# Kernel tuning notes

Hardware: AMD Instinct MI355X
Metric: run time of the kernel (lower is better)

## Reference

```python
import math
import jax, jax.numpy as jnp
import numpy as np

# ---- static configuration (mirrors init_kwargs / chosen shapes) ----
MUL = 16          # multiplicity in "16x0e+16x1e+16x2e"
B_CFG = 64        # number of configurations in batch
N_ATOM = 64       # atoms per configuration
N_NODES = B_CFG * N_ATOM
N_PAIRS = B_CFG * N_ATOM * N_ATOM

# ---- real Wigner 3j symbols (e3nn convention), computed once in numpy ----
def _su2_cg(j1, m1, j2, m2, j3, m3):
    if m3 != m1 + m2:
        return 0.0
    f = math.factorial
    vmin = max(-j1 + j2 + m3, -j1 + m1, 0)
    vmax = min(j2 + j3 + m1, j3 - j1 + j2, j3 + m3)
    C = math.sqrt((2 * j3 + 1) * f(j3 + j1 - j2) * f(j3 - j1 + j2) * f(j1 + j2 - j3)
                  * f(j3 + m3) * f(j3 - m3)
                  / (f(j1 + j2 + j3 + 1) * f(j1 - m1) * f(j1 + m1) * f(j2 - m2) * f(j2 + m2)))
    S = 0.0
    for v in range(vmin, vmax + 1):
        S += (-1) ** (v + j2 + m2) * f(j2 + j3 + m1 - v) * f(j1 - m1 + v) / (
            f(v) * f(j3 - j1 + j2 - v) * f(j3 + m3 - v) * f(v + j1 - j2 - m3))
    return C * S

def _q_real_to_complex(l):
    q = np.zeros((2 * l + 1, 2 * l + 1), dtype=np.complex128)
    for m in range(-l, 0):
        q[l + m, l + abs(m)] = 1 / 2 ** 0.5
        q[l + m, l - abs(m)] = -1j / 2 ** 0.5
    q[l, l] = 1.0
    for m in range(1, l + 1):
        q[l + m, l + abs(m)] = (-1) ** m / 2 ** 0.5
        q[l + m, l - abs(m)] = 1j * (-1) ** m / 2 ** 0.5
    return (-1j) ** l * q

def _wigner_3j(l1, l2, l3):
    C = np.zeros((2 * l1 + 1, 2 * l2 + 1, 2 * l3 + 1))
    for m1 in range(-l1, l1 + 1):
        for m2 in range(-l2, l2 + 1):
            m3 = m1 + m2
            if abs(m3) <= l3:
                C[l1 + m1, l2 + m2, l3 + m3] = _su2_cg(l1, m1, l2, m2, l3, m3)
    Q1, Q2, Q3 = _q_real_to_complex(l1), _q_real_to_complex(l2), _q_real_to_complex(l3)
    Cr = np.einsum('ij,kl,mn,ikm->jln', Q1, Q2, np.conj(Q3), C.astype(np.complex128))
    assert np.abs(Cr.imag).max() < 1e-6
    Cr = Cr.real
    return Cr / np.linalg.norm(Cr)

# all CG paths (l1, l2, l_out) of the fully connected TP (0e+1e+2e)^2 -> 0e+1e+2e
PATHS = [(0, 0, 0), (1, 1, 0), (2, 2, 0),
         (0, 1, 1), (1, 0, 1), (1, 1, 1), (1, 2, 1), (2, 1, 1), (2, 2, 1),
         (0, 2, 2), (2, 0, 2), (1, 1, 2), (1, 2, 2), (2, 1, 2), (2, 2, 2)]
W3J = {p: _wigner_3j(*p) for p in set(PATHS)}
FAN = {lo: sum(1 for p in PATHS if p[2] == lo) * MUL * MUL for lo in (0, 1, 2)}
ALPHA = {lo: math.sqrt(2 * lo + 1) / math.sqrt(FAN[lo]) for lo in (0, 1, 2)}
# CartesianTensor('ij=ij') change of basis: x_ij = sum_{l,m} QCART[lm,i,j] * irreps[lm]
QCART = np.concatenate([math.sqrt(2 * l + 1) * np.transpose(_wigner_3j(1, 1, l), (2, 0, 1))
                        for l in (0, 1, 2)], axis=0)  # (9, 3, 3), orthonormal rows


def setup_inputs() -> dict:
    key = jax.random.key(0)
    k1, k2 = jax.random.split(key)
    node_feats = jax.random.normal(k1, (N_NODES, MUL * 9), dtype=jnp.float32)
    # layout: for each config, all (i, j) atom pairs with global node indices
    ii, jj = jnp.meshgrid(jnp.arange(N_ATOM, dtype=jnp.int32),
                          jnp.arange(N_ATOM, dtype=jnp.int32), indexing='ij')
    base = (jnp.arange(B_CFG, dtype=jnp.int32) * N_ATOM)[:, None, None]
    rows = (base + ii[None]).reshape(-1)
    cols = (base + jj[None]).reshape(-1)
    layout = jnp.stack([rows, cols], axis=1)  # (N_PAIRS, 2) int32
    tp_weights = jax.random.normal(k2, (len(PATHS), MUL, MUL), dtype=jnp.float32)
    return {'node_feats': node_feats, 'layout': layout, 'tp_weights': tp_weights}


def _split(x):
    # (E, MUL*9) -> {l: (E, MUL, 2l+1)} in irreps order 16x0e | 16x1e | 16x2e
    E = x.shape[0]
    return {0: x[:, :MUL].reshape(E, MUL, 1),
            1: x[:, MUL:4 * MUL].reshape(E, MUL, 3),
            2: x[:, 4 * MUL:].reshape(E, MUL, 5)}


def _forward(node_feats, tp_weights, layout):
    x1 = _split(node_feats[layout[:, 0]])   # gather row atoms
    x2 = _split(node_feats[layout[:, 1]])   # gather column atoms
    E = layout.shape[0]
    dt = node_feats.dtype
    out = {lo: jnp.zeros((E, 2 * lo + 1), dt) for lo in (0, 1, 2)}
    for p, (l1, l2, lo) in enumerate(PATHS):
        w3j = jnp.asarray(W3J[(l1, l2, lo)], dt)
        t = jnp.einsum('eui,uv->evi', x1[l1], tp_weights[p])          # mix multiplicities
        out[lo] = out[lo] + ALPHA[lo] * jnp.einsum('evi,evj,ijk->ek', t, x2[l2], w3j)
    irr = jnp.concatenate([out[0], out[1], out[2]], axis=1)           # (E, 9) = 0e+1e+2e
    cart = jnp.einsum('ek,kij->eij', irr, jnp.asarray(QCART, dt))     # (E, 3, 3)
    # symmetrize: (H + H^T)/2 on the 3n x 3n per-config Hessian
    c = cart.reshape(B_CFG, N_ATOM, N_ATOM, 3, 3)
    c = 0.5 * (c + jnp.transpose(c, (0, 2, 1, 4, 3)))
    return c.reshape(E, 3, 3)


def reference(node_feats, layout, tp_weights):
    return _forward(node_feats, tp_weights, layout)
```

## Files before the change

kernel.cpp:

```cpp
#include <hip/hip_runtime.h>
#include <math.h>


#define NPATH 15

__constant__ int cP_L1[NPATH]   = {0,1,2,0,1,1,1,2,2,0,2,1,1,2,2};
__constant__ int cP_L2[NPATH]   = {0,1,2,1,0,1,2,1,2,2,0,1,2,1,2};
__constant__ int cP_LO[NPATH]   = {0,0,0,1,1,1,1,1,1,2,2,2,2,2,2};
__constant__ int cP_WOFF[NPATH] = {0,1,10,35,44,53,80,125,170,245,270,295,340,415,490};
__constant__ int cP_PROW[NPATH] = {0,1,10,35,38,41,50,65,80,105,110,115,124,139,164};
__constant__ int cC2P[51] = {0, 1,1,1, 2,2,2,2,2, 3, 4,4,4, 5,5,5, 6,6,6,
                             7,7,7,7,7, 8,8,8,8,8, 9, 10,10,10,10,10,
                             11,11,11, 12,12,12, 13,13,13,13,13, 14,14,14,14,14};
__constant__ int cC2I[51] = {0, 0,1,2, 0,1,2,3,4, 0, 0,1,2, 0,1,2, 0,1,2,
                             0,1,2,3,4, 0,1,2,3,4, 0, 0,1,2,3,4,
                             0,1,2, 0,1,2, 0,1,2,3,4, 0,1,2,3,4};

#define WS_B8   0
#define WS_B1   1512
#define WS_CR   2048

__device__ __forceinline__ double dfact(int n){
  double r = 1.0;
  for (int i = 2; i <= n; ++i) r *= (double)i;
  return r;
}

__device__ double su2_cg(int j1,int m1,int j2,int m2,int j3,int m3){
  if (m3 != m1 + m2) return 0.0;
  int vmin = -j1 + j2 + m3;
  if (-j1 + m1 > vmin) vmin = -j1 + m1;
  if (0 > vmin) vmin = 0;
  int vmax = j2 + j3 + m1;
  if (j3 - j1 + j2 < vmax) vmax = j3 - j1 + j2;
  if (j3 + m3 < vmax) vmax = j3 + m3;
  double C = sqrt((2.0*j3+1.0)*dfact(j3+j1-j2)*dfact(j3-j1+j2)*dfact(j1+j2-j3)
                  *dfact(j3+m3)*dfact(j3-m3)
                  /(dfact(j1+j2+j3+1)*dfact(j1-m1)*dfact(j1+m1)*dfact(j2-m2)*dfact(j2+m2)));
  double S = 0.0;
  for (int v = vmin; v <= vmax; ++v){
    double term = dfact(j2+j3+m1-v)*dfact(j1-m1+v)
                /(dfact(v)*dfact(j3-j1+j2-v)*dfact(j3+m3-v)*dfact(v+j1-j2-m3));
    S += ((v + j2 + m2) & 1) ? -term : term;
  }
  return C * S;
}

__device__ __forceinline__ void build_q(int l, double qre[5][5], double qim[5][5]){
  for (int r = 0; r < 5; ++r)
    for (int c = 0; c < 5; ++c){ qre[r][c] = 0.0; qim[r][c] = 0.0; }
  double s = 1.0 / sqrt(2.0);
  for (int m = -l; m < 0; ++m){
    qre[l+m][l-m] = s;
    qim[l+m][l+m] = -s;
  }
  qre[l][l] = 1.0;
  for (int m = 1; m <= l; ++m){
    double sgn = (m & 1) ? -1.0 : 1.0;
    qre[l+m][l+m] = sgn * s;
    qim[l+m][l-m] = sgn * s;
  }
  if (l == 1){
    for (int r = 0; r < 5; ++r)
      for (int c = 0; c < 5; ++c){
        double a = qre[r][c], b = qim[r][c];
        qre[r][c] = b; qim[r][c] = -a;
      }
  } else if (l == 2){
    for (int r = 0; r < 5; ++r)
      for (int c = 0; c < 5; ++c){ qre[r][c] = -qre[r][c]; qim[r][c] = -qim[r][c]; }
  }
}

__global__ __launch_bounds__(128) void initA_kernel(float* __restrict__ ws){
  __shared__ double sQre[3][5][5];
  __shared__ double sQim[3][5][5];
  __shared__ double sCG[125];
  __shared__ double sRed[128];
  const int p   = blockIdx.x;
  const int tid = threadIdx.x;
  const int l1 = cP_L1[p], l2 = cP_L2[p], l3 = cP_LO[p];
  const int d1 = 2*l1+1, d2 = 2*l2+1, d3 = 2*l3+1;

  if (tid < 3) build_q(tid, sQre[tid], sQim[tid]);

  if (tid < 125){
    int i = tid / 25, k = (tid / 5) % 5, m = tid % 5;
    double val = 0.0;
    if (i < d1 && k < d2 && m < d3)
      val = su2_cg(l1, i - l1, l2, k - l2, l3, m - l3);
    sCG[tid] = val;
  }
  __syncthreads();

  const int sz = d1 * d2 * d3;
  double acc = 0.0;
  if (tid < sz){
    int j = tid / (d2 * d3);
    int rem = tid - j * (d2 * d3);
    int l = rem / d3, n = rem - l * d3;
    for (int i = 0; i < d1; ++i)
      for (int k = 0; k < d2; ++k)
        for (int m = 0; m < d3; ++m){
          double c = sCG[(i*5 + k)*5 + m];
          if (c == 0.0) continue;
          double are = sQre[l1][i][j], aim = sQim[l1][i][j];
          double bre = sQre[l2][k][l], bim = sQim[l2][k][l];
          double tre = are*bre - aim*bim;
          double tim = are*bim + aim*bre;
          double cre = sQre[l3][m][n], cim = sQim[l3][m][n];
          acc += (tre*cre + tim*cim) * c;
        }
  }
  sRed[tid] = acc * acc;
  __syncthreads();
  for (int s = 64; s > 0; s >>= 1){
    if (tid < s) sRed[tid] += sRed[tid + s];
    __syncthreads();
  }
  double inv = 1.0 / sqrt(sRed[0]);
  double* crg = (double*)(ws + WS_CR);
  if (tid < sz) crg[cP_WOFF[p] + tid] = acc * inv;
}

__global__ __launch_bounds__(512) void initB_kernel(float* __restrict__ ws){
  __shared__ double sCr[615];
  __shared__ double sQCd[81];
  const int tid = threadIdx.x;
  const double* crg = (const double*)(ws + WS_CR);
  for (int t = tid; t < 615; t += 512) sCr[t] = crg[t];
  __syncthreads();

  if (tid < 81){
    int lm = tid / 9, r = tid - lm * 9;
    int l = (lm == 0) ? 0 : ((lm < 4) ? 1 : 2);
    int m = lm - l * l;
    int pq = (l == 0) ? 1 : ((l == 1) ? 5 : 11);
    sQCd[lm * 9 + r] = sCr[cP_WOFF[pq] + r * (2*l + 1) + m] * sqrt(2.0*l + 1.0);
  }
  __syncthreads();

  const double AL0 = 0.03608439182435161;
  const double AL1 = 0.04419417382415922;
  const double AL2 = 0.05705443310009863;
  for (int t = tid; t < NPATH * 225; t += 512){
    int p = t / 225, idx = t - p * 225;
    int i = idx / 45, j = (idx / 9) % 5, a = idx % 9;
    int d1 = 2*cP_L1[p]+1, d2 = 2*cP_L2[p]+1, d3 = 2*cP_LO[p]+1;
    if (i >= d1 || j >= d2) continue;
    int lo = cP_LO[p];
    double al = (lo == 0) ? AL0 : ((lo == 1) ? AL1 : AL2);
    double acc = 0.0;
    for (int m = 0; m < d3; ++m)
      acc += sCr[cP_WOFF[p] + (i*d2 + j)*d3 + m] * sQCd[(lo*lo + m)*9 + a];
    int row = cP_PROW[p] + i*d2 + j;
    float val = (float)(al * acc);
    if (a < 8) ws[WS_B8 + row*8 + a] = val;
    else       ws[WS_B1 + row]       = val;
  }
}

#define ACCP(TOFF_, PROW_, D1_)                                              \
  { _Pragma("unroll")                                                        \
    for (int i = 0; i < (D1_); ++i){                                         \
      float tv = pT[((TOFF_) + i) * 16 + v];                                 \
      int row = (PROW_) + i * D2 + j;                                        \
      const float4 m0 = *(const float4*)&sB8[row * 8];                       \
      const float4 m1 = *(const float4*)&sB8[row * 8 + 4];                   \
      const float  m8 = sB1[row];                                            \
      acc[0] += tv*m0.x; acc[1] += tv*m0.y; acc[2] += tv*m0.z;               \
      acc[3] += tv*m0.w; acc[4] += tv*m1.x; acc[5] += tv*m1.y;               \
      acc[6] += tv*m1.z; acc[7] += tv*m1.w; acc[8] += tv*m8;                 \
    } }

__global__ __launch_bounds__(256, 4) void fused_kernel(
    const float* __restrict__ feats,
    const int*   __restrict__ layout,
    const float* __restrict__ tpw,
    const float* __restrict__ ws,
    float*       __restrict__ out)
{
  __shared__ __align__(16) float sB8[189 * 8];
  __shared__ float sB1[192];
  __shared__ __align__(16) float sT[4][816];
  __shared__ __align__(16) float sMqT[4][1296];
  const int tid  = threadIdx.x;
  const int wave = tid >> 6;
  const int lane = tid & 63;

  for (int o = tid; o < 1512; o += 256) sB8[o] = ws[WS_B8 + o];
  if (tid < 189) sB1[tid] = ws[WS_B1 + tid];

  const int rw = blockIdx.x * 4 + wave;
  const int e0 = rw * 64;
  int rowNode = layout[2 * e0];
  rowNode = __builtin_amdgcn_readfirstlane(rowNode);
  const float* __restrict__ x1 = feats + (size_t)rowNode * 144;

  float* __restrict__ pT = sT[wave];
  {
    const int v  = lane & 15;
    const int cq = lane >> 4;
    for (int it = 0; it < 13; ++it){
      int c = cq + it * 4;
      if (c < 51){
        int p = cC2P[c], i = cC2I[c];
        int l1 = cP_L1[p];
        int st = 2*l1 + 1;
        int loff = (l1 == 0) ? 0 : ((l1 == 1) ? 16 : 64);
        const float* xb = x1 + loff + i;
        const float* wb = tpw + p * 256 + v;
        float s = 0.f;
        #pragma unroll
        for (int u = 0; u < 16; ++u) s += xb[u * st] * wb[u * 16];
        pT[c * 16 + v] = s;
      }
    }
  }

  __syncthreads();

  float* __restrict__ pM = sMqT[wave];
  for (int rnd = 0; rnd < 3; ++rnd){
    int c = lane + rnd * 64;
    if (c >= 144) break;
    float acc[9];
    #pragma unroll
    for (int a = 0; a < 9; ++a) acc[a] = 0.f;
    if (c < 16){
      const int v = c, j = 0;
      const int D2 = 1;
      ACCP(0,  0,   1)
      ACCP(10, 38,  3)
      ACCP(30, 110, 5)
    } else if (c < 64){
      const int v = (c - 16) / 3, j = (c - 16) % 3;
      const int D2 = 3;
      ACCP(1,  1,   3)
      ACCP(9,  35,  1)
      ACCP(13, 41,  3)
      ACCP(19, 65,  5)
      ACCP(35, 115, 3)
      ACCP(41, 139, 5)
    } else {
      const int v = (c - 64) / 5, j = (c - 64) % 5;
      const int D2 = 5;
      ACCP(4,  10,  5)
      ACCP(16, 50,  3)
      ACCP(24, 80,  5)
      ACCP(29, 105, 1)
      ACCP(38, 124, 3)
      ACCP(46, 164, 5)
    }
    #pragma unroll
    for (int a = 0; a < 9; ++a) pM[a * 144 + c] = acc[a];
  }

  const size_t e = (size_t)e0 + lane;
  const int col = layout[2 * e + 1];
  const float* __restrict__ x2 = feats + (size_t)col * 144;

  float acc[9];
  #pragma unroll
  for (int a = 0; a < 9; ++a) acc[a] = 0.f;

  for (int cc = 0; cc < 36; ++cc){
    const float4 x = *(const float4*)(x2 + cc * 4);
    const float* mb = pM + cc * 4;
    #pragma unroll
    for (int a = 0; a < 9; ++a){
      float4 m = *(const float4*)(mb + a * 144);
      acc[a] += x.x*m.x + x.y*m.y + x.z*m.z + x.w*m.w;
    }
  }

  #pragma unroll
  for (int a = 0; a < 9; ++a) pT[lane * 9 + a] = acc[a];
  float* ob = out + (size_t)e0 * 9;
  #pragma unroll
  for (int r = 0; r < 3; ++r){
    int idx = lane + r * 64;
    if (idx < 144){
      float4 vv = *(const float4*)(pT + idx * 4);
      *(float4*)(ob + idx * 4) = vv;
    }
  }
}

__global__ __launch_bounds__(256) void sym_kernel(float* __restrict__ out, int total){
  int o = blockIdx.x * 256 + threadIdx.x;
  if (o >= total) return;
  int e = o / 9;
  int r = o - e * 9;
  int a = r / 3, d = r - a * 3;
  int i = (e >> 6) & 63;
  int j = e & 63;
  bool active = (i < j) || (i == j && a < d);
  if (!active) return;
  int e2 = (e & ~4095) | (j << 6) | i;
  int o2 = e2 * 9 + d * 3 + a;
  float v = 0.5f * (out[o] + out[o2]);
  out[o]  = v;
  out[o2] = v;
}

extern "C" void kernel_launch(void* const* d_in, const int* in_sizes, int n_in,
                              void* d_out, int out_size, void* d_ws, size_t ws_size,
                              hipStream_t stream) {
  const float* feats  = (const float*)d_in[0];
  const int*   layout = (const int*)  d_in[1];
  const float* tpw    = (const float*)d_in[2];
  float* out = (float*)d_out;
  float* ws  = (float*)d_ws;

  const int E = in_sizes[1] / 2;
  const int R = E / 64;

  initA_kernel<<<NPATH, 128, 0, stream>>>(ws);
  initB_kernel<<<1, 512, 0, stream>>>(ws);
  fused_kernel<<<R / 4, 256, 0, stream>>>(feats, layout, tpw, ws, out);
  sym_kernel<<<(E * 9 + 255) / 256, 256, 0, stream>>>(out, E * 9);
}
```

Measured before the change: 133.9 us.

## Split fused kernel into per-row matrix and contraction kernels, tile symmetrization

Splits the fused kernel in two when workspace allows. The first kernel builds the per-row-atom contraction matrix and writes it to global workspace; the second contracts that matrix with the column atom features and writes the Cartesian blocks. The old per-element symmetrization, with its scattered transpose reads, is replaced by a shared-memory tiled kernel that loads 16x16 atom-pair tiles and their transposed partners together, so global accesses are coalesced. The split adds a global round-trip of the intermediate matrix and one extra launch, but each kernel may reach higher occupancy.

Result: slower. 172.8 us (+29.1%).

```diff
diff --git a/kernel.cpp b/kernel.cpp
--- a/kernel.cpp
+++ b/kernel.cpp
@@ -19,6 +19,8 @@
 #define WS_B8   0
 #define WS_B1   1512
 #define WS_CR   2048
+#define WS_MQ   2048
+#define MQ_STRIDE 1296
 
 __device__ __forceinline__ double dfact(int n){
   double r = 1.0;
@@ -173,12 +175,12 @@
       acc[6] += tv*m1.z; acc[7] += tv*m1.w; acc[8] += tv*m8;                 \
     } }
 
-__global__ __launch_bounds__(256, 4) void fused_kernel(
+__global__ __launch_bounds__(256, 4) void mq_kernel(
     const float* __restrict__ feats,
     const int*   __restrict__ layout,
     const float* __restrict__ tpw,
     const float* __restrict__ ws,
-    float*       __restrict__ out)
+    float*       __restrict__ mqg)
 {
   __shared__ __align__(16) float sB8[189 * 8];
   __shared__ float sB1[192];
@@ -192,8 +194,7 @@
   if (tid < 189) sB1[tid] = ws[WS_B1 + tid];
 
   const int rw = blockIdx.x * 4 + wave;
-  const int e0 = rw * 64;
-  int rowNode = layout[2 * e0];
+  int rowNode = layout[2 * (rw * 64)];
   rowNode = __builtin_amdgcn_readfirstlane(rowNode);
   const float* __restrict__ x1 = feats + (size_t)rowNode * 144;
 
@@ -256,6 +257,144 @@
     for (int a = 0; a < 9; ++a) pM[a * 144 + c] = acc[a];
   }
 
+  float* __restrict__ dst = mqg + (size_t)rw * MQ_STRIDE;
+  #pragma unroll
+  for (int r = 0; r < 6; ++r){
+    int idx = lane + r * 64;
+    if (idx < 324){
+      float4 vv = *(const float4*)(pM + idx * 4);
+      *(float4*)(dst + idx * 4) = vv;
+    }
+  }
+}
+
+__global__ __launch_bounds__(256) void cart_kernel(
+    const float* __restrict__ feats,
+    const int*   __restrict__ layout,
+    const float* __restrict__ mqg,
+    float*       __restrict__ out)
+{
+  __shared__ __align__(16) float sOut[4][576];
+  const int tid  = threadIdx.x;
+  const int wave = tid >> 6;
+  const int lane = tid & 63;
+  const int rw = blockIdx.x * 4 + wave;
+
+  const float* __restrict__ m = mqg + (size_t)rw * MQ_STRIDE;
+  const size_t e = (size_t)rw * 64 + lane;
+  const int col = layout[2 * e + 1];
+  const float* __restrict__ x2 = feats + (size_t)col * 144;
+
+  float acc[9];
+  #pragma unroll
+  for (int a = 0; a < 9; ++a) acc[a] = 0.f;
+
+  for (int cc = 0; cc < 36; ++cc){
+    const float4 x = *(const float4*)(x2 + cc * 4);
+    const float* mb = m + cc * 4;
+    #pragma unroll
+    for (int a = 0; a < 9; ++a){
+      float4 mm = *(const float4*)(mb + a * 144);
+      acc[a] += x.x*mm.x + x.y*mm.y + x.z*mm.z + x.w*mm.w;
+    }
+  }
+
+  float* __restrict__ pO = sOut[wave];
+  #pragma unroll
+  for (int a = 0; a < 9; ++a) pO[lane * 9 + a] = acc[a];
+  float* __restrict__ ob = out + (size_t)rw * 576;
+  #pragma unroll
+  for (int r = 0; r < 3; ++r){
+    int idx = lane + r * 64;
+    if (idx < 144){
+      float4 vv = *(const float4*)(pO + idx * 4);
+      *(float4*)(ob + idx * 4) = vv;
+    }
+  }
+}
+
+__global__ __launch_bounds__(256, 4) void fused_kernel(
+    const float* __restrict__ feats,
+    const int*   __restrict__ layout,
+    const float* __restrict__ tpw,
+    const float* __restrict__ ws,
+    float*       __restrict__ out)
+{
+  __shared__ __align__(16) float sB8[189 * 8];
+  __shared__ float sB1[192];
+  __shared__ __align__(16) float sT[4][816];
+  __shared__ __align__(16) float sMqT[4][1296];
+  const int tid  = threadIdx.x;
+  const int wave = tid >> 6;
+  const int lane = tid & 63;
+
+  for (int o = tid; o < 1512; o += 256) sB8[o] = ws[WS_B8 + o];
+  if (tid < 189) sB1[tid] = ws[WS_B1 + tid];
+
+  const int rw = blockIdx.x * 4 + wave;
+  const int e0 = rw * 64;
+  int rowNode = layout[2 * e0];
+  rowNode = __builtin_amdgcn_readfirstlane(rowNode);
+  const float* __restrict__ x1 = feats + (size_t)rowNode * 144;
+
+  float* __restrict__ pT = sT[wave];
+  {
+    const int v  = lane & 15;
+    const int cq = lane >> 4;
+    for (int it = 0; it < 13; ++it){
+      int c = cq + it * 4;
+      if (c < 51){
+        int p = cC2P[c], i = cC2I[c];
+        int l1 = cP_L1[p];
+        int st = 2*l1 + 1;
+        int loff = (l1 == 0) ? 0 : ((l1 == 1) ? 16 : 64);
+        const float* xb = x1 + loff + i;
+        const float* wb = tpw + p * 256 + v;
+        float s = 0.f;
+        #pragma unroll
+        for (int u = 0; u < 16; ++u) s += xb[u * st] * wb[u * 16];
+        pT[c * 16 + v] = s;
+      }
+    }
+  }
+  __syncthreads();
+
+  float* __restrict__ pM = sMqT[wave];
+  for (int rnd = 0; rnd < 3; ++rnd){
+    int c = lane + rnd * 64;
+    if (c >= 144) break;
+    float acc[9];
+    #pragma unroll
+    for (int a = 0; a < 9; ++a) acc[a] = 0.f;
+    if (c < 16){
+      const int v = c, j = 0;
+      const int D2 = 1;
+      ACCP(0,  0,   1)
+      ACCP(10, 38,  3)
+      ACCP(30, 110, 5)
+    } else if (c < 64){
+      const int v = (c - 16) / 3, j = (c - 16) % 3;
+      const int D2 = 3;
+      ACCP(1,  1,   3)
+      ACCP(9,  35,  1)
+      ACCP(13, 41,  3)
+      ACCP(19, 65,  5)
+      ACCP(35, 115, 3)
+      ACCP(41, 139, 5)
+    } else {
+      const int v = (c - 64) / 5, j = (c - 64) % 5;
+      const int D2 = 5;
+      ACCP(4,  10,  5)
+      ACCP(16, 50,  3)
+      ACCP(24, 80,  5)
+      ACCP(29, 105, 1)
+      ACCP(38, 124, 3)
+      ACCP(46, 164, 5)
+    }
+    #pragma unroll
+    for (int a = 0; a < 9; ++a) pM[a * 144 + c] = acc[a];
+  }
+
   const size_t e = (size_t)e0 + lane;
   const int col = layout[2 * e + 1];
   const float* __restrict__ x2 = feats + (size_t)col * 144;
@@ -269,8 +408,8 @@
     const float* mb = pM + cc * 4;
     #pragma unroll
     for (int a = 0; a < 9; ++a){
-      float4 m = *(const float4*)(mb + a * 144);
-      acc[a] += x.x*m.x + x.y*m.y + x.z*m.z + x.w*m.w;
+      float4 mv = *(const float4*)(mb + a * 144);
+      acc[a] += x.x*mv.x + x.y*mv.y + x.z*mv.z + x.w*mv.w;
     }
   }
 
@@ -287,21 +426,62 @@
   }
 }
 
-__global__ __launch_bounds__(256) void sym_kernel(float* __restrict__ out, int total){
-  int o = blockIdx.x * 256 + threadIdx.x;
-  if (o >= total) return;
-  int e = o / 9;
-  int r = o - e * 9;
-  int a = r / 3, d = r - a * 3;
-  int i = (e >> 6) & 63;
-  int j = e & 63;
-  bool active = (i < j) || (i == j && a < d);
-  if (!active) return;
-  int e2 = (e & ~4095) | (j << 6) | i;
-  int o2 = e2 * 9 + d * 3 + a;
-  float v = 0.5f * (out[o] + out[o2]);
-  out[o]  = v;
-  out[o2] = v;
+__global__ __launch_bounds__(256) void sym_tiled(float* __restrict__ out){
+  __shared__ float sA[16 * 145];
+  __shared__ float sB[16 * 145];
+  const int tid = threadIdx.x;
+  const int b  = blockIdx.x / 10;
+  const int tp = blockIdx.x - b * 10;
+  const int TI[10] = {0,0,0,0,1,1,1,2,2,3};
+  const int TJ[10] = {0,1,2,3,1,2,3,2,3,3};
+  const int ti = TI[tp], tj = TJ[tp];
+  const bool diag = (ti == tj);
+  const size_t cfgBase = (size_t)b * 4096 * 9;
+
+  for (int idx = tid; idx < 2304; idx += 256){
+    int r = idx / 144, off = idx - r * 144;
+    sA[r * 145 + off] = out[cfgBase + ((size_t)(ti*16 + r) * 64 + tj*16) * 9 + off];
+  }
+  if (!diag){
+    for (int idx = tid; idx < 2304; idx += 256){
+      int r = idx / 144, off = idx - r * 144;
+      sB[r * 145 + off] = out[cfgBase + ((size_t)(tj*16 + r) * 64 + ti*16) * 9 + off];
+    }
+  }
+  __syncthreads();
+
+  const int di = tid >> 4, dj = tid & 15;
+  const float* A = sA;
+  const float* B = diag ? sA : sB;
+  float oa[9], ob[9];
+  #pragma unroll
+  for (int a = 0; a < 3; ++a)
+    #pragma unroll
+    for (int d = 0; d < 3; ++d){
+      oa[a*3+d] = 0.5f * (A[di*145 + dj*9 + a*3+d] + B[dj*145 + di*9 + d*3+a]);
+      if (!diag)
+        ob[a*3+d] = 0.5f * (B[di*145 + dj*9 + a*3+d] + A[dj*145 + di*9 + d*3+a]);
+    }
+  __syncthreads();
+
+  #pragma unroll
+  for (int r9 = 0; r9 < 9; ++r9) sA[di*145 + dj*9 + r9] = oa[r9];
+  if (!diag){
+    #pragma unroll
+    for (int r9 = 0; r9 < 9; ++r9) sB[di*145 + dj*9 + r9] = ob[r9];
+  }
+  __syncthreads();
+
+  for (int idx = tid; idx < 2304; idx += 256){
+    int r = idx / 144, off = idx - r * 144;
+    out[cfgBase + ((size_t)(ti*16 + r) * 64 + tj*16) * 9 + off] = sA[r * 145 + off];
+  }
+  if (!diag){
+    for (int idx = tid; idx < 2304; idx += 256){
+      int r = idx / 144, off = idx - r * 144;
+      out[cfgBase + ((size_t)(tj*16 + r) * 64 + ti*16) * 9 + off] = sB[r * 145 + off];
+    }
+  }
 }
 
 extern "C" void kernel_launch(void* const* d_in, const int* in_sizes, int n_in,
@@ -315,9 +495,18 @@
 
   const int E = in_sizes[1] / 2;
   const int R = E / 64;
+  const int B = E / 4096;
 
   initA_kernel<<<NPATH, 128, 0, stream>>>(ws);
   initB_kernel<<<1, 512, 0, stream>>>(ws);
-  fused_kernel<<<R / 4, 256, 0, stream>>>(feats, layout, tpw, ws, out);
-  sym_kernel<<<(E * 9 + 255) / 256, 256, 0, stream>>>(out, E * 9);
-}
+
+  const size_t need = ((size_t)WS_MQ + (size_t)R * MQ_STRIDE) * sizeof(float);
+  if (ws_size >= need){
+    float* mqg = ws + WS_MQ;
+    mq_kernel  <<<R / 4, 256, 0, stream>>>(feats, layout, tpw, ws, mqg);
+    cart_kernel<<<R / 4, 256, 0, stream>>>(feats, layout, mqg, out);
+  } else {
+    fused_kernel<<<R / 4, 256, 0, stream>>>(feats, layout, tpw, ws, out);
+  }
+  sym_tiled<<<B * 10, 256, 0, stream>>>(out);
+}
```
